# Kernel tuning notes

Measured on AMD Instinct MI355X. Metric: run time of the kernel, lower is better.

Reference implementation:

```python
import jax, jax.numpy as jnp
import numpy as np

B, S, HID = 4, 1024, 1024
NH = 16
DH = HID // NH  # 64


def _split_heads(t):
    # [B, S, HID] -> [B, NH, S, DH]
    return t.reshape(B, S, NH, DH).transpose(0, 2, 1, 3)


def _merge_heads(t):
    # [B, NH, S, DH] -> [B, S, HID]
    return t.transpose(0, 2, 1, 3).reshape(B, S, HID)


def setup_inputs() -> dict:
    key = jax.random.key(0)
    ks = jax.random.split(key, 13)
    scale = 1.0 / np.sqrt(HID)
    inp = {"x": jax.random.normal(ks[0], (B, S, HID), dtype=jnp.float32)}
    names = ["Wq", "Wk", "Wv", "Wq2", "Wk2", "Wv2"]
    for i, n in enumerate(names):
        inp[n] = jax.random.normal(ks[1 + i], (HID, HID), dtype=jnp.float32) * scale
        inp["b" + n[1:]] = jax.random.normal(ks[7 + i], (HID,), dtype=jnp.float32) * 0.01
    return inp


def _attn(q, k, v):
    # q,k,v: [B, NH, S, DH]
    scores = jnp.einsum("bhqd,bhkd->bhqk", q, k) / np.sqrt(DH).astype(np.float32)
    probs = jax.nn.softmax(scores, axis=-1)
    return jnp.einsum("bhqk,bhkd->bhqd", probs, v)


def reference(x, Wq, bq, Wk, bk, Wv, bv, Wq2, bq2, Wk2, bk2, Wv2, bv2):
    # nn.Linear: y = x @ W.T + b
    q1 = _split_heads(x @ Wq.T + bq)
    k1 = _split_heads(x @ Wk.T + bk)
    v1 = _split_heads(x @ Wv.T + bv)
    q2 = _split_heads(x @ Wq2.T + bq2)
    k2 = _split_heads(x @ Wk2.T + bk2)
    v2 = _split_heads(x @ Wv2.T + bv2)
    # 5'UTR direction: q1 attends to k2/v2; 3'UTR direction: q2 attends to k1/v1
    out5 = _merge_heads(_attn(q1, k2, v2))
    out3 = _merge_heads(_attn(q2, k1, v1))
    return (out5, out3)
```

## Files before the change

kernel.cpp:

```cpp
#include <hip/hip_runtime.h>


typedef __attribute__((ext_vector_type(8))) short bf16x8;
typedef __attribute__((ext_vector_type(4))) short bf16x4;
typedef __attribute__((ext_vector_type(4))) float f32x4;
typedef __attribute__((ext_vector_type(4))) short s16x4;

#define MFMA16(a, b, c) __builtin_amdgcn_mfma_f32_16x16x32_bf16(a, b, c, 0, 0, 0)
#define BARRIER() asm volatile("s_barrier" ::: "memory")
#define VMCNT0() asm volatile("s_waitcnt vmcnt(0)" ::: "memory")

__device__ __forceinline__ f32x4 mfma16k(bf16x4 a, bf16x4 b, f32x4 c) {
#if __has_builtin(__builtin_amdgcn_mfma_f32_16x16x16bf16_1k)
  return __builtin_amdgcn_mfma_f32_16x16x16bf16_1k(a, b, c, 0, 0, 0);
#elif __has_builtin(__builtin_amdgcn_mfma_f32_16x16x16_bf16)
  return __builtin_amdgcn_mfma_f32_16x16x16_bf16(a, b, c, 0, 0, 0);
#else
  asm volatile("v_mfma_f32_16x16x16_bf16 %0, %1, %2, %0"
               : "+v"(c) : "v"(a), "v"(b));
  return c;
#endif
}

__device__ __forceinline__ unsigned short f2bf(float f) {
  unsigned u = __float_as_uint(f);
  u = (u + 0x7fffu + ((u >> 16) & 1u)) >> 16;
  return (unsigned short)u;
}

__device__ __forceinline__ unsigned cvt_pk_bf16(float lo, float hi) {
  unsigned r;
  asm("v_cvt_pk_bf16_f32 %0, %1, %2" : "=v"(r) : "v"(lo), "v"(hi));
  return r;
}

__device__ __forceinline__ void gll16(const void* g, void* l) {
  __builtin_amdgcn_global_load_lds(
      (const __attribute__((address_space(1))) unsigned int*)g,
      (__attribute__((address_space(3))) unsigned int*)l, 16, 0, 0);
}

__global__ __launch_bounds__(256) void convert_k(
    const float* __restrict__ x,
    const float* __restrict__ W0, const float* __restrict__ W1,
    const float* __restrict__ W2, const float* __restrict__ W3,
    const float* __restrict__ W4, const float* __restrict__ W5,
    short* __restrict__ xbf, short* __restrict__ wbf) {
  const int total = (10 << 20) >> 2;
  for (int tid = blockIdx.x * 256 + threadIdx.x; tid < total;
       tid += 2048 * 256) {
    const int e = tid << 2;
    const float* src;
    short* dst;
    int off;
    if (e < (4 << 20)) {
      src = x; dst = xbf; off = e;
    } else {
      const int j = e - (4 << 20);
      const int wsel = j >> 20;
      off = j & ((1 << 20) - 1);
      src = (wsel == 0) ? W0 : (wsel == 1) ? W1 : (wsel == 2) ? W2
          : (wsel == 3) ? W3 : (wsel == 4) ? W4 : W5;
      dst = wbf + ((size_t)wsel << 20);
    }
    const float4 v = *(const float4*)(src + off);
    s16x4 o;
    o.x = (short)f2bf(v.x);
    o.y = (short)f2bf(v.y);
    o.z = (short)f2bf(v.z);
    o.w = (short)f2bf(v.w);
    *(s16x4*)(dst + off) = o;
  }
}

__global__ __launch_bounds__(512, 2) void proj_gemm192(
    const short* __restrict__ Ag, const short* __restrict__ Wall,
    const float* __restrict__ bq, const float* __restrict__ bk,
    const float* __restrict__ bv, const float* __restrict__ bq2,
    const float* __restrict__ bk2, const float* __restrict__ bv2,
    short* __restrict__ qkv) {
  __shared__ __align__(16) short As[2][16384];
  __shared__ __align__(16) short Bs[2][12288];

  const int bid = blockIdx.x;
  const int xcd = bid & 7, k = bid >> 3;
  const int ns = k & 3, mb = k >> 2;
  const int nbase = (xcd * 4 + ns) * 192;
  const int m0 = mb << 8;

  const int t = threadIdx.x, lane = t & 63, w = t >> 6;
  const int g = lane >> 4, lr = lane & 15;
  const int wr = w >> 2, wc = w & 3;

  f32x4 acc[2][4][3] = {};

  auto stage_ah = [&](int T, int H) {
#pragma unroll
    for (int ld = 0; ld < 2; ++ld) {
      const int slot = (H << 10) + (ld << 9) + t;
      const int rr = slot >> 3;
      const int gc = (slot & 7) ^ (rr & 7);
      gll16(Ag + (size_t)(m0 + rr) * 1024 + (T << 6) + (gc << 3),
            &As[T & 1][slot * 8]);
    }
  };
  auto stage_b = [&](int T) {
#pragma unroll
    for (int ld = 0; ld < 3; ++ld) {
      const int slot = (ld << 9) + t;
      const int rr = slot >> 3;
      const int gc = (slot & 7) ^ (rr & 7);
      gll16(Wall + (size_t)(nbase + rr) * 1024 + (T << 6) + (gc << 3),
            &Bs[T & 1][slot * 8]);
    }
  };

  stage_ah(0, 0); stage_ah(0, 1); stage_b(0);
  VMCNT0();
  BARRIER();

#define LOAD_A(AV, MH, KK, TB)                                            \
  _Pragma("unroll") for (int mi = 0; mi < 4; ++mi) {                      \
    const int rA = wr * 128 + (MH) * 64 + mi * 16 + lr;                   \
    AV[mi] = *(const bf16x8*)                                             \
        &As[TB][rA * 64 + ((((KK) * 4 + g) ^ (rA & 7)) << 3)];            \
  }
#define LOAD_B(KK, TB)                                                    \
  _Pragma("unroll") for (int nj = 0; nj < 3; ++nj) {                      \
    const int rB = wc * 48 + nj * 16 + lr;                                \
    bf[nj] = *(const bf16x8*)                                             \
        &Bs[TB][rB * 64 + ((((KK) * 4 + g) ^ (rB & 7)) << 3)];            \
  }
#define MFMA_MH(MH, AV)                                                   \
  _Pragma("unroll") for (int mi = 0; mi < 4; ++mi)                        \
    _Pragma("unroll") for (int nj = 0; nj < 3; ++nj)                      \
      acc[MH][mi][nj] = MFMA16(AV[mi], bf[nj], acc[MH][mi][nj]);

  auto group = [&](int C, int TD, bool DV) {
    bf16x8 af0[4], af1[4], bf[3];
    {
      LOAD_A(af0, 0, 0, C); LOAD_A(af1, 1, 0, C); LOAD_B(0, C);
      if (DV) { stage_ah(TD, 0); stage_ah(TD, 1); }
      BARRIER();
      __builtin_amdgcn_s_setprio(1);
      MFMA_MH(0, af0);
      MFMA_MH(1, af1);
      __builtin_amdgcn_s_setprio(0);
      BARRIER();
    }
    {
      LOAD_A(af0, 0, 1, C); LOAD_A(af1, 1, 1, C); LOAD_B(1, C);
      if (DV) stage_b(TD);
      BARRIER();
      __builtin_amdgcn_s_setprio(1);
      MFMA_MH(0, af0);
      MFMA_MH(1, af1);
      __builtin_amdgcn_s_setprio(0);
      VMCNT0();
      BARRIER();
    }
  };

  for (int j = 0; j < 8; ++j) {
    group(0, 2 * j + 1, true);
    group(1, 2 * j + 2, j < 7);
  }

#undef LOAD_A
#undef LOAD_B
#undef MFMA_MH

#pragma unroll
  for (int nj = 0; nj < 3; ++nj) {
    const int nn = nbase + wc * 48 + nj * 16 + lr;
    const int p = nn >> 10, nl = nn & 1023;
    const float* bp = (p == 0) ? bq : (p == 1) ? bk : (p == 2) ? bv
                    : (p == 3) ? bq2 : (p == 4) ? bk2 : bv2;
    const float bb = bp[nl];
    const int h = nl >> 6, d = nl & 63;
    const int pt = (p == 0 || p == 3) ? 0 : (p == 1 || p == 4) ? 1 : 2;
    unsigned short* dst = (unsigned short*)qkv + ((size_t)p << 22);
#pragma unroll
    for (int mh = 0; mh < 2; ++mh) {
#pragma unroll
      for (int mi = 0; mi < 4; ++mi) {
#pragma unroll
        for (int r = 0; r < 4; ++r) {
          const int m = m0 + wr * 128 + mh * 64 + mi * 16 + (g << 2) + r;
          const int b = m >> 10, s = m & 1023;
          const unsigned short val = f2bf(acc[mh][mi][nj][r] + bb);
          size_t idx;
          if (pt == 0) {
            idx = ((size_t)(((b << 4) + h) * 1024 + s) << 6) + d;
          } else if (pt == 1) {
            const int d2 = (d & 7) | (((d >> 3) ^ (s & 7)) << 3);
            idx = ((size_t)(((b << 4) + h) * 1024 + s) << 6) + d2;
          } else {
            const int tt = s >> 6, s2 = s & 63;
            const int s3 = (s2 & 7) | (((s2 >> 3) ^ (d & 7)) << 3);
            idx = ((size_t)((((b << 4) + h) * 16 + tt) * 64 + d) << 6) + s3;
          }
          dst[idx] = val;
        }
      }
    }
  }
}

__global__ __launch_bounds__(512) void attn_k(const short* __restrict__ qkv,
                                              float* __restrict__ out) {
  __shared__ __align__(16) short Ks[2][64 * 64];
  __shared__ __align__(16) short Vs[2][64 * 64];

  const int L = blockIdx.x;
  const int xcd = L & 7, ss = L >> 3;
  const int qt = ss & 7, pg = ss >> 3;
  const int pp = xcd + (pg << 3);
  const int hb = pp & 63, dir = pp >> 6;

  const short* Q = qkv + ((size_t)(dir ? 3 : 0) << 22) + ((size_t)hb << 16);
  const short* K = qkv + ((size_t)(dir ? 1 : 4) << 22) + ((size_t)hb << 16);
  const short* V = qkv + ((size_t)(dir ? 2 : 5) << 22) + ((size_t)hb << 16);
  float* O = out + ((size_t)dir << 22);

  const int t = threadIdx.x, lane = t & 63, w = t >> 6;
  const int g = lane >> 4, lr = lane & 15;

  const int qrow = (qt << 7) + (w << 4) + lr;
  bf16x8 qf[2];
  qf[0] = *(const bf16x8*)(Q + qrow * 64 + g * 8);
  qf[1] = *(const bf16x8*)(Q + qrow * 64 + 32 + g * 8);

  const bf16x4 ones4 = {0x3F80, 0x3F80, 0x3F80, 0x3F80};

  f32x4 oacc[4] = {};
  f32x4 lacc = {};
  float mrun = -3.0e38f;
  const float CSC = 0.18033688f;

  const int srow = t >> 3;
  const int scol = (t & 7) << 3;

  auto stage = [&](int kt, int buf) {
    gll16(K + (size_t)((kt << 6) + srow) * 64 + scol, &Ks[buf][w << 9]);
    gll16(V + (size_t)(kt << 12) + (size_t)srow * 64 + scol, &Vs[buf][w << 9]);
  };

  auto tile = [&](int kt, auto curc) {
    constexpr int CUR = decltype(curc)::value;
    if (kt < 15) stage(kt + 1, CUR ^ 1);

    f32x4 sc2[4] = {};
    __builtin_amdgcn_s_setprio(1);
#pragma unroll
    for (int dk = 0; dk < 2; ++dk) {
#pragma unroll
      for (int kn = 0; kn < 4; ++kn) {
        const int krow = kn * 16 + lr;
        const bf16x8 kf = *(const bf16x8*)
            &Ks[CUR][krow * 64 +
                     ((((dk << 6) + (g << 4)) ^ ((krow & 7) << 4)) >> 1)];
        sc2[kn] = MFMA16(kf, qf[dk], sc2[kn]);
      }
    }
    __builtin_amdgcn_s_setprio(0);

    float tm = fmaxf(fmaxf(fmaxf(sc2[0][0], sc2[0][1]),
                           fmaxf(sc2[0][2], sc2[0][3])),
                     fmaxf(fmaxf(sc2[1][0], sc2[1][1]),
                           fmaxf(sc2[1][2], sc2[1][3])));
    tm = fmaxf(tm, fmaxf(fmaxf(fmaxf(sc2[2][0], sc2[2][1]),
                               fmaxf(sc2[2][2], sc2[2][3])),
                         fmaxf(fmaxf(sc2[3][0], sc2[3][1]),
                               fmaxf(sc2[3][2], sc2[3][3]))));
    const bool ok = __all(fmaf(tm, CSC, -mrun) <= 8.0f);
    if (!ok) {
      float t2 = fmaxf(tm, __shfl_xor(tm, 16));
      t2 = fmaxf(t2, __shfl_xor(t2, 32));
      const float mnew = fmaxf(mrun, t2 * CSC);
      const float scq = exp2f(mrun - mnew);
      mrun = mnew;
#pragma unroll
      for (int r = 0; r < 4; ++r) {
        const float sr = __shfl(scq, (g << 2) + r);
        lacc[r] *= sr;
#pragma unroll
        for (int dn = 0; dn < 4; ++dn) oacc[dn][r] *= sr;
      }
    }

    bf16x4 pa[4];
#pragma unroll
    for (int kn = 0; kn < 4; ++kn) {
      const float p0 = exp2f(fmaf(sc2[kn][0], CSC, -mrun));
      const float p1 = exp2f(fmaf(sc2[kn][1], CSC, -mrun));
      const float p2 = exp2f(fmaf(sc2[kn][2], CSC, -mrun));
      const float p3 = exp2f(fmaf(sc2[kn][3], CSC, -mrun));
      union { unsigned u[2]; bf16x4 v; } pk;
      pk.u[0] = cvt_pk_bf16(p0, p1);
      pk.u[1] = cvt_pk_bf16(p2, p3);
      pa[kn] = pk.v;
    }

    __builtin_amdgcn_s_setprio(1);
#pragma unroll
    for (int kn = 0; kn < 4; ++kn) {
      lacc = mfma16k(pa[kn], ones4, lacc);
#pragma unroll
      for (int dn = 0; dn < 4; ++dn) {
        const int vrow = dn * 16 + lr;
        const int ch = (2 * kn + (g >> 1)) ^ (vrow & 7);
        const bf16x4 vf = *(const bf16x4*)
            &Vs[CUR][vrow * 64 + ch * 8 + ((g & 1) << 2)];
        oacc[dn] = mfma16k(pa[kn], vf, oacc[dn]);
      }
    }
    __builtin_amdgcn_s_setprio(0);

    VMCNT0();
    BARRIER();
  };

  stage(0, 0);
  VMCNT0();
  BARRIER();

#pragma unroll
  for (int kp = 0; kp < 8; ++kp) {
    tile(2 * kp, std::integral_constant<int, 0>{});
    tile(2 * kp + 1, std::integral_constant<int, 1>{});
  }

  const int b = hb >> 4, h = hb & 15;
  float rl[4];
#pragma unroll
  for (int r = 0; r < 4; ++r) rl[r] = 1.0f / lacc[r];
#pragma unroll
  for (int dn = 0; dn < 4; ++dn) {
#pragma unroll
    for (int r = 0; r < 4; ++r) {
      const int q = (qt << 7) + (w << 4) + (g << 2) + r;
      const int d = dn * 16 + lr;
      O[((size_t)(b * 1024 + q) << 10) + h * 64 + d] = oacc[dn][r] * rl[r];
    }
  }
}

extern "C" void kernel_launch(void* const* d_in, const int* in_sizes, int n_in,
                              void* d_out, int out_size, void* d_ws,
                              size_t ws_size, hipStream_t stream) {
  const float* x   = (const float*)d_in[0];
  const float* Wq  = (const float*)d_in[1];
  const float* bq  = (const float*)d_in[2];
  const float* Wk  = (const float*)d_in[3];
  const float* bk  = (const float*)d_in[4];
  const float* Wv  = (const float*)d_in[5];
  const float* bv  = (const float*)d_in[6];
  const float* Wq2 = (const float*)d_in[7];
  const float* bq2 = (const float*)d_in[8];
  const float* Wk2 = (const float*)d_in[9];
  const float* bk2 = (const float*)d_in[10];
  const float* Wv2 = (const float*)d_in[11];
  const float* bv2 = (const float*)d_in[12];

  char* ws = (char*)d_ws;
  short* xbf = (short*)ws;
  short* wbf = (short*)(ws + 8388608);
  short* qkv = (short*)(ws + 20971520);

  convert_k<<<2048, 256, 0, stream>>>(x, Wq, Wk, Wv, Wq2, Wk2, Wv2, xbf, wbf);
  proj_gemm192<<<512, 512, 0, stream>>>(xbf, wbf, bq, bk, bv, bq2, bk2,
                                        bv2, qkv);
  attn_k<<<1024, 512, 0, stream>>>(qkv, (float*)d_out);
}
```

Measured before the change: 153.0 us.

## Retile projection GEMM to 128x192 blocks with 256 threads and more blocks

The projection GEMM tile drops from 256x192 with 512 threads to 128x192 with 256 threads, and the grid doubles to 1024 blocks. Each wave now computes a 64x96 sub-tile (4x6 MFMAs) instead of 128x48, which changes the A/B fragment reuse ratio. Block index mapping is reordered so consecutive blocks on an XCD share the same N slice. The intent is better occupancy and load balance across CUs. The cost is lower arithmetic intensity per block and more redundant loads of the B operand.

```diff
diff --git a/kernel.cpp b/kernel.cpp
--- a/kernel.cpp
+++ b/kernel.cpp
@@ -73,31 +73,31 @@
   }
 }
 
-__global__ __launch_bounds__(512, 2) void proj_gemm192(
+__global__ __launch_bounds__(256, 2) void proj_t2(
     const short* __restrict__ Ag, const short* __restrict__ Wall,
     const float* __restrict__ bq, const float* __restrict__ bk,
     const float* __restrict__ bv, const float* __restrict__ bq2,
     const float* __restrict__ bk2, const float* __restrict__ bv2,
     short* __restrict__ qkv) {
-  __shared__ __align__(16) short As[2][16384];
+  __shared__ __align__(16) short As[2][8192];
   __shared__ __align__(16) short Bs[2][12288];
 
   const int bid = blockIdx.x;
-  const int xcd = bid & 7, k = bid >> 3;
-  const int ns = k & 3, mb = k >> 2;
+  const int xcd = bid & 7, i = bid >> 3;
+  const int ns = i >> 5, mb = i & 31;
   const int nbase = (xcd * 4 + ns) * 192;
-  const int m0 = mb << 8;
+  const int m0 = mb << 7;
 
   const int t = threadIdx.x, lane = t & 63, w = t >> 6;
   const int g = lane >> 4, lr = lane & 15;
-  const int wr = w >> 2, wc = w & 3;
-
-  f32x4 acc[2][4][3] = {};
-
-  auto stage_ah = [&](int T, int H) {
-#pragma unroll
-    for (int ld = 0; ld < 2; ++ld) {
-      const int slot = (H << 10) + (ld << 9) + t;
+  const int wr = w >> 1, wc = w & 1;
+
+  f32x4 acc[4][6] = {};
+
+  auto stage_a = [&](int T) {
+#pragma unroll
+    for (int ld = 0; ld < 4; ++ld) {
+      const int slot = (ld << 8) + t;
       const int rr = slot >> 3;
       const int gc = (slot & 7) ^ (rr & 7);
       gll16(Ag + (size_t)(m0 + rr) * 1024 + (T << 6) + (gc << 3),
@@ -106,8 +106,8 @@
   };
   auto stage_b = [&](int T) {
 #pragma unroll
-    for (int ld = 0; ld < 3; ++ld) {
-      const int slot = (ld << 9) + t;
+    for (int ld = 0; ld < 6; ++ld) {
+      const int slot = (ld << 8) + t;
       const int rr = slot >> 3;
       const int gc = (slot & 7) ^ (rr & 7);
       gll16(Wall + (size_t)(nbase + rr) * 1024 + (T << 6) + (gc << 3),
@@ -115,64 +115,57 @@
     }
   };
 
-  stage_ah(0, 0); stage_ah(0, 1); stage_b(0);
+  stage_a(0); stage_b(0);
   VMCNT0();
   BARRIER();
 
-#define LOAD_A(AV, MH, KK, TB)                                            \
+#define LOAD_A(KK, TB)                                                    \
   _Pragma("unroll") for (int mi = 0; mi < 4; ++mi) {                      \
-    const int rA = wr * 128 + (MH) * 64 + mi * 16 + lr;                   \
-    AV[mi] = *(const bf16x8*)                                             \
+    const int rA = wr * 64 + mi * 16 + lr;                                \
+    af[mi] = *(const bf16x8*)                                             \
         &As[TB][rA * 64 + ((((KK) * 4 + g) ^ (rA & 7)) << 3)];            \
   }
 #define LOAD_B(KK, TB)                                                    \
-  _Pragma("unroll") for (int nj = 0; nj < 3; ++nj) {                      \
-    const int rB = wc * 48 + nj * 16 + lr;                                \
+  _Pragma("unroll") for (int nj = 0; nj < 6; ++nj) {                      \
+    const int rB = wc * 96 + nj * 16 + lr;                                \
     bf[nj] = *(const bf16x8*)                                             \
         &Bs[TB][rB * 64 + ((((KK) * 4 + g) ^ (rB & 7)) << 3)];            \
   }
-#define MFMA_MH(MH, AV)                                                   \
+#define MFMA_C()                                                          \
+  __builtin_amdgcn_s_setprio(1);                                          \
   _Pragma("unroll") for (int mi = 0; mi < 4; ++mi)                        \
-    _Pragma("unroll") for (int nj = 0; nj < 3; ++nj)                      \
-      acc[MH][mi][nj] = MFMA16(AV[mi], bf[nj], acc[MH][mi][nj]);
-
-  auto group = [&](int C, int TD, bool DV) {
-    bf16x8 af0[4], af1[4], bf[3];
+    _Pragma("unroll") for (int nj = 0; nj < 6; ++nj)                      \
+      acc[mi][nj] = MFMA16(af[mi], bf[nj], acc[mi][nj]);                  \
+  __builtin_amdgcn_s_setprio(0);
+
+  for (int T = 0; T < 16; ++T) {
+    const int C = T & 1;
+    const bool DV = T < 15;
+    bf16x8 af[4], bf[6];
     {
-      LOAD_A(af0, 0, 0, C); LOAD_A(af1, 1, 0, C); LOAD_B(0, C);
-      if (DV) { stage_ah(TD, 0); stage_ah(TD, 1); }
+      LOAD_A(0, C); LOAD_B(0, C);
+      if (DV) stage_a(T + 1);
       BARRIER();
-      __builtin_amdgcn_s_setprio(1);
-      MFMA_MH(0, af0);
-      MFMA_MH(1, af1);
-      __builtin_amdgcn_s_setprio(0);
+      MFMA_C();
       BARRIER();
     }
     {
-      LOAD_A(af0, 0, 1, C); LOAD_A(af1, 1, 1, C); LOAD_B(1, C);
-      if (DV) stage_b(TD);
+      LOAD_A(1, C); LOAD_B(1, C);
+      if (DV) stage_b(T + 1);
       BARRIER();
-      __builtin_amdgcn_s_setprio(1);
-      MFMA_MH(0, af0);
-      MFMA_MH(1, af1);
-      __builtin_amdgcn_s_setprio(0);
+      MFMA_C();
       VMCNT0();
       BARRIER();
     }
-  };
-
-  for (int j = 0; j < 8; ++j) {
-    group(0, 2 * j + 1, true);
-    group(1, 2 * j + 2, j < 7);
   }
 
 #undef LOAD_A
 #undef LOAD_B
-#undef MFMA_MH
-
-#pragma unroll
-  for (int nj = 0; nj < 3; ++nj) {
-    const int nn = nbase + wc * 48 + nj * 16 + lr;
+#undef MFMA_C
+
+#pragma unroll
+  for (int nj = 0; nj < 6; ++nj) {
+    const int nn = nbase + wc * 96 + nj * 16 + lr;
     const int p = nn >> 10, nl = nn & 1023;
     const float* bp = (p == 0) ? bq : (p == 1) ? bk : (p == 2) ? bv
                     : (p == 3) ? bq2 : (p == 4) ? bk2 : bv2;
@@ -181,27 +174,24 @@
     const int pt = (p == 0 || p == 3) ? 0 : (p == 1 || p == 4) ? 1 : 2;
     unsigned short* dst = (unsigned short*)qkv + ((size_t)p << 22);
 #pragma unroll
-    for (int mh = 0; mh < 2; ++mh) {
-#pragma unroll
-      for (int mi = 0; mi < 4; ++mi) {
-#pragma unroll
-        for (int r = 0; r < 4; ++r) {
-          const int m = m0 + wr * 128 + mh * 64 + mi * 16 + (g << 2) + r;
-          const int b = m >> 10, s = m & 1023;
-          const unsigned short val = f2bf(acc[mh][mi][nj][r] + bb);
-          size_t idx;
-          if (pt == 0) {
-            idx = ((size_t)(((b << 4) + h) * 1024 + s) << 6) + d;
-          } else if (pt == 1) {
-            const int d2 = (d & 7) | (((d >> 3) ^ (s & 7)) << 3);
-            idx = ((size_t)(((b << 4) + h) * 1024 + s) << 6) + d2;
-          } else {
-            const int tt = s >> 6, s2 = s & 63;
-            const int s3 = (s2 & 7) | (((s2 >> 3) ^ (d & 7)) << 3);
-            idx = ((size_t)((((b << 4) + h) * 16 + tt) * 64 + d) << 6) + s3;
-          }
-          dst[idx] = val;
+    for (int mi = 0; mi < 4; ++mi) {
+#pragma unroll
+      for (int r = 0; r < 4; ++r) {
+        const int m = m0 + wr * 64 + mi * 16 + (g << 2) + r;
+        const int b = m >> 10, s = m & 1023;
+        const unsigned short val = f2bf(acc[mi][nj][r] + bb);
+        size_t idx;
+        if (pt == 0) {
+          idx = ((size_t)(((b << 4) + h) * 1024 + s) << 6) + d;
+        } else if (pt == 1) {
+          const int d2 = (d & 7) | (((d >> 3) ^ (s & 7)) << 3);
+          idx = ((size_t)(((b << 4) + h) * 1024 + s) << 6) + d2;
+        } else {
+          const int tt = s >> 6, s2 = s & 63;
+          const int s3 = (s2 & 7) | (((s2 >> 3) ^ (d & 7)) << 3);
+          idx = ((size_t)((((b << 4) + h) * 16 + tt) * 64 + d) << 6) + s3;
         }
+        dst[idx] = val;
       }
     }
   }
@@ -369,7 +359,7 @@
   short* qkv = (short*)(ws + 20971520);
 
   convert_k<<<2048, 256, 0, stream>>>(x, Wq, Wk, Wv, Wq2, Wk2, Wv2, xbf, wbf);
-  proj_gemm192<<<512, 512, 0, stream>>>(xbf, wbf, bq, bk, bv, bq2, bk2,
-                                        bv2, qkv);
+  proj_t2<<<1024, 256, 0, stream>>>(xbf, wbf, bq, bk, bv, bq2, bk2,
+                                    bv2, qkv);
   attn_k<<<1024, 512, 0, stream>>>(qkv, (float*)d_out);
 }
```

Result: faster. 149.5 us (-2.3%).
